# Optimization experiments

Measured on AMD Instinct MI355X. Metric: run time of the kernel, lower is better.

Reference implementation:

```python
import jax, jax.numpy as jnp
import numpy as np
from jax.scipy.special import logsumexp

EPS = 0.05        # entropic regularization (blur^p)
N_ITERS = 20      # Sinkhorn iterations
N, M, D = 8192, 8192, 64


def setup_inputs() -> dict:
    key = jax.random.key(0)
    k1, k2, k3, k4 = jax.random.split(key, 4)
    return {
        "a": jax.random.uniform(k1, (N,), dtype=jnp.float32),
        "x": jax.random.normal(k2, (N, D), dtype=jnp.float32),
        "b": jax.random.uniform(k3, (M,), dtype=jnp.float32),
        "y": jax.random.normal(k4, (M, D), dtype=jnp.float32),
    }


def reference(a, x, b, y):
    eps = EPS
    # _normalize_weights: probability simplex
    a = a / jnp.sum(a)
    b = b / jnp.sum(b)
    loga = jnp.log(a)
    logb = jnp.log(b)
    # squared-Euclidean cost C_ij = ||x_i - y_j||^2, built via one GEMM (online kernel's math)
    x2 = jnp.sum(x * x, axis=1)            # [N]
    y2 = jnp.sum(y * y, axis=1)            # [M]
    C = x2[:, None] + y2[None, :] - 2.0 * (x @ y.T)   # [N, M]

    # log-domain Sinkhorn: f_i = -eps * LSE_j( log b_j + (g_j - C_ij)/eps )
    def softmin_rows(g_, C_, logw):   # reduce over columns j -> [N]
        return -eps * logsumexp(logw[None, :] + (g_[None, :] - C_) / eps, axis=1)

    def softmin_cols(f_, C_, logw):   # reduce over rows i -> [M]
        return -eps * logsumexp(logw[:, None] + (f_[:, None] - C_) / eps, axis=0)

    def body(i, fg):
        f_, g_ = fg
        f_ = softmin_rows(g_, C, logb)
        g_ = softmin_cols(f_, C, loga)
        return (f_, g_)

    f0 = jnp.zeros_like(a)
    g0 = jnp.zeros_like(b)
    f, g = jax.lax.fori_loop(0, N_ITERS, body, (f0, g0))

    # GeomLoss-style: one final symmetric update from detached potentials (Danskin)
    f_d = jax.lax.stop_gradient(f)
    g_d = jax.lax.stop_gradient(g)
    f_fin = softmin_rows(g_d, C, logb)
    g_fin = softmin_cols(f_d, C, loga)
    # OT_eps(a, b) = <a, f> + <b, g>
    return jnp.sum(a * f_fin) + jnp.sum(b * g_fin)
```

## Files before the change

### kernel.cpp

```cpp
#include <hip/hip_runtime.h>
#include <hip/hip_bf16.h>

#define EPS       0.05f
#define N_ITERS   20
#define NR        8192
#define DIM       64
#define LOG2E     1.4426950408889634f
#define LN2       0.6931471805599453f
#define S2        (2.0f * LOG2E / EPS)
#define EPSLN2    (EPS * LN2)
#define NEGINF    (-1e30f)
#define NSPLIT    4

typedef __attribute__((ext_vector_type(8))) short short8;
typedef __attribute__((ext_vector_type(4))) float float4v;

__device__ __forceinline__ float wave_reduce_sum(float v) {
    #pragma unroll
    for (int m = 1; m < 64; m <<= 1) v += __shfl_xor(v, m, 64);
    return v;
}

__device__ __forceinline__ float merge4_l(float2 p0, float2 p1, float2 p2, float2 p3) {
    float M = fmaxf(fmaxf(p0.x, p1.x), fmaxf(p2.x, p3.x));
    float S = p0.y * __builtin_amdgcn_exp2f(p0.x - M)
            + p1.y * __builtin_amdgcn_exp2f(p1.x - M)
            + p2.y * __builtin_amdgcn_exp2f(p2.x - M)
            + p3.y * __builtin_amdgcn_exp2f(p3.x - M);
    return M + __builtin_amdgcn_logf(S);
}

__global__ void sums_kernel(const float* __restrict__ a, const float* __restrict__ b,
                            float* __restrict__ sums) {
    __shared__ float red[32];
    int tid = threadIdx.x;
    float pa = 0.f, pb = 0.f;
    for (int i = tid; i < NR; i += blockDim.x) { pa += a[i]; pb += b[i]; }
    pa = wave_reduce_sum(pa);
    pb = wave_reduce_sum(pb);
    int wid = tid >> 6, ln = tid & 63;
    if (ln == 0) { red[wid] = pa; red[wid + 16] = pb; }
    __syncthreads();
    if (tid == 0) {
        float sa = 0.f, sb = 0.f;
        int nw = blockDim.x >> 6;
        for (int w = 0; w < nw; w++) { sa += red[w]; sb += red[w + 16]; }
        sums[0] = logf(sa); sums[1] = logf(sb); sums[2] = sa; sums[3] = sb;
    }
}

__global__ void prep_kernel(const float* __restrict__ x, const float* __restrict__ y,
                            const float* __restrict__ a, const float* __restrict__ b,
                            const float* __restrict__ sums,
                            short8* __restrict__ xr, short8* __restrict__ yr,
                            short8* __restrict__ xs, short8* __restrict__ ys,
                            float* __restrict__ x2, float* __restrict__ y2,
                            float* __restrict__ la2, float* __restrict__ lb2,
                            float2* __restrict__ Pb) {
    int gid = blockIdx.x * 256 + threadIdx.x;
    bool isx = gid < NR * 8;
    int cid = isx ? gid : gid - NR * 8;
    int row = cid >> 3;
    int c   = cid & 7;
    const float4* src = (const float4*)(isx ? x : y);
    float4 v0 = src[row * 16 + c * 2];
    float4 v1 = src[row * 16 + c * 2 + 1];

    short8 st;
    st[0] = __bfloat16_as_short(__float2bfloat16(v0.x));
    st[1] = __bfloat16_as_short(__float2bfloat16(v0.y));
    st[2] = __bfloat16_as_short(__float2bfloat16(v0.z));
    st[3] = __bfloat16_as_short(__float2bfloat16(v0.w));
    st[4] = __bfloat16_as_short(__float2bfloat16(v1.x));
    st[5] = __bfloat16_as_short(__float2bfloat16(v1.y));
    st[6] = __bfloat16_as_short(__float2bfloat16(v1.z));
    st[7] = __bfloat16_as_short(__float2bfloat16(v1.w));

    (isx ? xr : yr)[row * 8 + c] = st;
    int T = row >> 4, ln = row & 15, f = c >> 2, q = c & 3;
    (isx ? xs : ys)[T * 128 + f * 64 + q * 16 + ln] = st;

    float sq = v0.x*v0.x + v0.y*v0.y + v0.z*v0.z + v0.w*v0.w
             + v1.x*v1.x + v1.y*v1.y + v1.z*v1.z + v1.w*v1.w;
    #pragma unroll
    for (int m = 1; m < 8; m <<= 1) sq += __shfl_xor(sq, m, 64);

    if (c == 0) {
        if (isx) {
            x2[row] = sq;
            la2[row] = (logf(a[row]) - sums[0]) * LOG2E;
        } else {
            y2[row] = sq;
            lb2[row] = (logf(b[row]) - sums[1]) * LOG2E;
            Pb[row] = make_float2(sq * (LOG2E / EPS), 1.0f);
            #pragma unroll
            for (int k = 1; k < NSPLIT; k++)
                Pb[k * NR + row] = make_float2(NEGINF, 0.0f);
        }
    }
}

#define LSE4(acc, c4, mm, ss)                                            \
    {                                                                    \
        float z0 = fmaf(S2, (acc)[0], (c4).x);                           \
        float z1 = fmaf(S2, (acc)[1], (c4).y);                           \
        float z2 = fmaf(S2, (acc)[2], (c4).z);                           \
        float z3 = fmaf(S2, (acc)[3], (c4).w);                           \
        float zm = fmaxf(fmaxf(z0, z1), fmaxf(z2, z3));                  \
        float mn = fmaxf((mm), zm);                                      \
        float e  = __builtin_amdgcn_exp2f((mm) - mn);                    \
        float p  = (__builtin_amdgcn_exp2f(z0 - mn)                      \
                  + __builtin_amdgcn_exp2f(z1 - mn))                     \
                 + (__builtin_amdgcn_exp2f(z2 - mn)                      \
                  + __builtin_amdgcn_exp2f(z3 - mn));                    \
        (ss) = fmaf((ss), e, p);                                         \
        (mm) = mn;                                                       \
    }

__global__ __launch_bounds__(1024, 4) void pass_kernel(
        const short8* __restrict__ matXr,
        const short8* __restrict__ matYs,
        const float2* __restrict__ Pin,
        const float* __restrict__ lw2col,
        float2* __restrict__ Pout) {
    __shared__ __attribute__((aligned(16))) char ybuf[2][32768];
    __shared__ __attribute__((aligned(16))) float cbl[2048];
    __shared__ float2 comb[128][9];

    const int tid = threadIdx.x;
    const int bi  = blockIdx.x;
    const int q4  = bi & 3;
    const int rb  = (bi >> 2) * 128;
    const int cb0 = q4 * 2048;

    {
        int j = cb0 + tid * 2;
        float4 p0 = *(const float4*)(Pin + 0 * NR + j);
        float4 p1 = *(const float4*)(Pin + 1 * NR + j);
        float4 p2 = *(const float4*)(Pin + 2 * NR + j);
        float4 p3 = *(const float4*)(Pin + 3 * NR + j);
        float2 lw = *(const float2*)(lw2col + j);
        float2 cb;
        cb.x = lw.x - merge4_l(make_float2(p0.x, p0.y), make_float2(p1.x, p1.y),
                               make_float2(p2.x, p2.y), make_float2(p3.x, p3.y));
        cb.y = lw.y - merge4_l(make_float2(p0.z, p0.w), make_float2(p1.z, p1.w),
                               make_float2(p2.z, p2.w), make_float2(p3.z, p3.w));
        *(float2*)(cbl + tid * 2) = cb;
    }

    const int w    = tid >> 6;
    const int lane = tid & 63;
    const int quad = lane >> 4;
    const int ln   = lane & 15;
    const int cs   = w & 7;
    const int rh   = w >> 3;

    short8 xf0[4], xf1[4];
    #pragma unroll
    for (int t = 0; t < 4; t++) {
        int r = rb + rh * 64 + t * 16 + ln;
        xf0[t] = matXr[r * 8 + quad];
        xf1[t] = matXr[r * 8 + quad + 4];
    }

    const char* ysrc = (const char*)matYs + (size_t)cb0 * 128;
    const int s0 = (bi >> 2) & 7;

    {
        const char* src = ysrc + s0 * 32768 + tid * 16;
        char* dst = &ybuf[0][(tid >> 6) * 1024];
        __builtin_amdgcn_global_load_lds(
            (const __attribute__((address_space(1))) void*)src,
            (__attribute__((address_space(3))) void*)dst, 16, 0, 0);
        __builtin_amdgcn_global_load_lds(
            (const __attribute__((address_space(1))) void*)(src + 16384),
            (__attribute__((address_space(3))) void*)(dst + 16384), 16, 0, 0);
    }

    float lm[4], ls[4];
    #pragma unroll
    for (int t = 0; t < 4; t++) { lm[t] = NEGINF; ls[t] = 0.f; }

    for (int t = 0; t < 8; t++) {
        const int cur = t & 1;
        const int sc  = (s0 + t) & 7;

        __builtin_amdgcn_s_waitcnt(0x0070);
        __builtin_amdgcn_s_barrier();
        __builtin_amdgcn_sched_barrier(0);

        if (t < 7) {
            const int sn = (s0 + t + 1) & 7;
            const char* src = ysrc + sn * 32768 + tid * 16;
            char* dst = &ybuf[1 - cur][(tid >> 6) * 1024];
            __builtin_amdgcn_global_load_lds(
                (const __attribute__((address_space(1))) void*)src,
                (__attribute__((address_space(3))) void*)dst, 16, 0, 0);
            __builtin_amdgcn_global_load_lds(
                (const __attribute__((address_space(1))) void*)(src + 16384),
                (__attribute__((address_space(3))) void*)(dst + 16384), 16, 0, 0);
        }
        __builtin_amdgcn_sched_barrier(0);

        const char* base = &ybuf[cur][0];
        #pragma unroll
        for (int uu = 0; uu < 2; uu++) {
            const int u = 2 * cs + uu;
            short8 ya0 = *(const short8*)(base + u * 2048 + lane * 16);
            short8 ya1 = *(const short8*)(base + u * 2048 + 1024 + lane * 16);
            float4 c4  = *(const float4*)(cbl + sc * 256 + u * 16 + quad * 4);

            float4v acc[4];
            #pragma unroll
            for (int tt = 0; tt < 4; tt++) {
                float4v z = {0.f, 0.f, 0.f, 0.f};
                z = __builtin_amdgcn_mfma_f32_16x16x32_bf16(ya0, xf0[tt], z, 0, 0, 0);
                z = __builtin_amdgcn_mfma_f32_16x16x32_bf16(ya1, xf1[tt], z, 0, 0, 0);
                acc[tt] = z;
            }
            #pragma unroll
            for (int tt = 0; tt < 4; tt++) LSE4(acc[tt], c4, lm[tt], ls[tt]);
        }
    }

    #pragma unroll
    for (int mask = 16; mask < 64; mask <<= 1) {
        #pragma unroll
        for (int t = 0; t < 4; t++) {
            float mo = __shfl_xor(lm[t], mask, 64);
            float so = __shfl_xor(ls[t], mask, 64);
            float M  = fmaxf(lm[t], mo);
            ls[t] = ls[t] * __builtin_amdgcn_exp2f(lm[t] - M)
                  + so    * __builtin_amdgcn_exp2f(mo    - M);
            lm[t] = M;
        }
    }

    if (lane < 16) {
        #pragma unroll
        for (int t = 0; t < 4; t++)
            comb[rh * 64 + t * 16 + ln][cs] = make_float2(lm[t], ls[t]);
    }
    __syncthreads();

    if (tid < 128) {
        float2 c = comb[tid][0];
        float M = c.x, S = c.y;
        #pragma unroll
        for (int cc = 1; cc < 8; cc++) {
            float2 p = comb[tid][cc];
            float Mn = fmaxf(M, p.x);
            S = S * __builtin_amdgcn_exp2f(M - Mn)
              + p.y * __builtin_amdgcn_exp2f(p.x - Mn);
            M = Mn;
        }
        Pout[q4 * NR + rb + tid] = make_float2(M, S);
    }
}

__global__ void reduce_kernel(const float* __restrict__ a, const float* __restrict__ b,
                              const float* __restrict__ sums,
                              const float* __restrict__ x2, const float* __restrict__ y2,
                              const float2* __restrict__ Pff, const float2* __restrict__ Pgf,
                              float* __restrict__ out) {
    __shared__ float red[32];
    int tid = threadIdx.x;
    float da = 0.f, db = 0.f;
    for (int i = tid; i < NR; i += blockDim.x) {
        float fv = x2[i] - EPSLN2 * merge4_l(Pff[i], Pff[NR + i],
                                             Pff[2 * NR + i], Pff[3 * NR + i]);
        float gv = y2[i] - EPSLN2 * merge4_l(Pgf[i], Pgf[NR + i],
                                             Pgf[2 * NR + i], Pgf[3 * NR + i]);
        da += a[i] * fv;
        db += b[i] * gv;
    }
    da = wave_reduce_sum(da);
    db = wave_reduce_sum(db);
    int wid = tid >> 6, ln = tid & 63;
    if (ln == 0) { red[wid] = da; red[wid + 16] = db; }
    __syncthreads();
    if (tid == 0) {
        float DA = 0.f, DB = 0.f;
        int nw = blockDim.x >> 6;
        for (int w = 0; w < nw; w++) { DA += red[w]; DB += red[w + 16]; }
        out[0] = DA / sums[2] + DB / sums[3];
    }
}

extern "C" void kernel_launch(void* const* d_in, const int* in_sizes, int n_in,
                              void* d_out, int out_size, void* d_ws, size_t ws_size,
                              hipStream_t stream) {
    const float* a = (const float*)d_in[0];
    const float* x = (const float*)d_in[1];
    const float* b = (const float*)d_in[2];
    const float* y = (const float*)d_in[3];

    char* ws = (char*)d_ws;
    short8* xr = (short8*)ws;
    short8* yr = (short8*)(ws + (1 << 20));
    short8* xs = (short8*)(ws + (2 << 20));
    short8* ys = (short8*)(ws + (3 << 20));
    float* fp  = (float*)(ws + (4 << 20));
    float* x2  = fp;
    float* y2  = fp + NR;
    float* la2 = fp + 2 * NR;
    float* lb2 = fp + 3 * NR;
    float2* P   = (float2*)(fp + 4 * NR);
    float2* Pf  = P;
    float2* Pb  = P + NSPLIT * NR;
    float2* Pff = P + 2 * NSPLIT * NR;
    float2* Pgf = P + 3 * NSPLIT * NR;
    float* sums = (float*)(P + 4 * NSPLIT * NR);

    sums_kernel<<<1, 1024, 0, stream>>>(a, b, sums);
    prep_kernel<<<(2 * NR * 8) / 256, 256, 0, stream>>>(x, y, a, b, sums,
                                                        xr, yr, xs, ys,
                                                        x2, y2, la2, lb2, Pb);

    for (int it = 0; it < N_ITERS; it++) {
        pass_kernel<<<256, 1024, 0, stream>>>(xr, ys, Pb, lb2, Pf);
        pass_kernel<<<256, 1024, 0, stream>>>(yr, xs, Pf, la2, Pb);
    }
    pass_kernel<<<256, 1024, 0, stream>>>(xr, ys, Pb, lb2, Pff);
    pass_kernel<<<256, 1024, 0, stream>>>(yr, xs, Pf, la2, Pgf);

    reduce_kernel<<<1, 1024, 0, stream>>>(a, b, sums, x2, y2, Pff, Pgf, (float*)d_out);
}
```

Measured before the change: 974.1 us.

## Retile pass kernel to 256-row blocks with 8-way column split and triple-buffered Y

Each pass block now covers 256 rows and a 1024-column slice, giving an 8-way column split instead of 4. This doubles the X-fragment reuse per wave and halves the Y bytes staged per step, and the Y loads become a three-deep LDS ring with one load kept in flight. The work is meant to raise MFMA work per LDS read and to hide global-load latency better. In exchange it costs more registers (8 row tiles of accumulators and LSE state) and doubles the partial-LSE merge work, both in the pass prologue and in the final reduce. The host launch grid is not shown and must match the new block count.

New measurement: 1.160 ms. +19.1%, slower.

```diff
diff --git a/kernel.cpp b/kernel.cpp
--- a/kernel.cpp
+++ b/kernel.cpp
@@ -10,24 +10,20 @@
 #define S2        (2.0f * LOG2E / EPS)
 #define EPSLN2    (EPS * LN2)
 #define NEGINF    (-1e30f)
-#define NSPLIT    4
+#define NSPLIT    8
 
 typedef __attribute__((ext_vector_type(8))) short short8;
 typedef __attribute__((ext_vector_type(4))) float float4v;
 
+#define GLD_LDS16(src, dst)                                              \
+    __builtin_amdgcn_global_load_lds(                                    \
+        (const __attribute__((address_space(1))) void*)(src),            \
+        (__attribute__((address_space(3))) void*)(dst), 16, 0, 0)
+
 __device__ __forceinline__ float wave_reduce_sum(float v) {
     #pragma unroll
     for (int m = 1; m < 64; m <<= 1) v += __shfl_xor(v, m, 64);
     return v;
-}
-
-__device__ __forceinline__ float merge4_l(float2 p0, float2 p1, float2 p2, float2 p3) {
-    float M = fmaxf(fmaxf(p0.x, p1.x), fmaxf(p2.x, p3.x));
-    float S = p0.y * __builtin_amdgcn_exp2f(p0.x - M)
-            + p1.y * __builtin_amdgcn_exp2f(p1.x - M)
-            + p2.y * __builtin_amdgcn_exp2f(p2.x - M)
-            + p3.y * __builtin_amdgcn_exp2f(p3.x - M);
-    return M + __builtin_amdgcn_logf(S);
 }
 
 __global__ void sums_kernel(const float* __restrict__ a, const float* __restrict__ b,
@@ -123,30 +119,16 @@
         const float2* __restrict__ Pin,
         const float* __restrict__ lw2col,
         float2* __restrict__ Pout) {
-    __shared__ __attribute__((aligned(16))) char ybuf[2][32768];
-    __shared__ __attribute__((aligned(16))) float cbl[2048];
-    __shared__ float2 comb[128][9];
+    __shared__ __attribute__((aligned(16))) char ybuf[3][16384];
+    __shared__ __attribute__((aligned(16))) float cbl[1024];
+    __shared__ float2 comb[256][9];
 
     const int tid = threadIdx.x;
     const int bi  = blockIdx.x;
-    const int q4  = bi & 3;
-    const int rb  = (bi >> 2) * 128;
-    const int cb0 = q4 * 2048;
-
-    {
-        int j = cb0 + tid * 2;
-        float4 p0 = *(const float4*)(Pin + 0 * NR + j);
-        float4 p1 = *(const float4*)(Pin + 1 * NR + j);
-        float4 p2 = *(const float4*)(Pin + 2 * NR + j);
-        float4 p3 = *(const float4*)(Pin + 3 * NR + j);
-        float2 lw = *(const float2*)(lw2col + j);
-        float2 cb;
-        cb.x = lw.x - merge4_l(make_float2(p0.x, p0.y), make_float2(p1.x, p1.y),
-                               make_float2(p2.x, p2.y), make_float2(p3.x, p3.y));
-        cb.y = lw.y - merge4_l(make_float2(p0.z, p0.w), make_float2(p1.z, p1.w),
-                               make_float2(p2.z, p2.w), make_float2(p3.z, p3.w));
-        *(float2*)(cbl + tid * 2) = cb;
-    }
+    const int q8  = bi & 7;
+    const int rg  = bi >> 3;
+    const int rb  = rg * 256;
+    const int cb0 = q8 * 1024;
 
     const int w    = tid >> 6;
     const int lane = tid & 63;
@@ -155,78 +137,76 @@
     const int cs   = w & 7;
     const int rh   = w >> 3;
 
-    short8 xf0[4], xf1[4];
-    #pragma unroll
-    for (int t = 0; t < 4; t++) {
-        int r = rb + rh * 64 + t * 16 + ln;
+    const char* ysrc = (const char*)matYs + (size_t)cb0 * 128;
+    const int c0 = rg & 7;
+
+    GLD_LDS16(ysrc + c0 * 16384 + w * 1024 + lane * 16, &ybuf[0][w * 1024]);
+    __builtin_amdgcn_sched_barrier(0);
+
+    {
+        int j = cb0 + tid;
+        float2 p[NSPLIT];
+        float M = NEGINF;
+        #pragma unroll
+        for (int k = 0; k < NSPLIT; k++) {
+            p[k] = Pin[k * NR + j];
+            M = fmaxf(M, p[k].x);
+        }
+        float S = 0.f;
+        #pragma unroll
+        for (int k = 0; k < NSPLIT; k++)
+            S += p[k].y * __builtin_amdgcn_exp2f(p[k].x - M);
+        cbl[tid] = lw2col[j] - (M + __builtin_amdgcn_logf(S));
+    }
+
+    short8 xf0[8], xf1[8];
+    #pragma unroll
+    for (int t = 0; t < 8; t++) {
+        int r = rb + rh * 128 + t * 16 + ln;
         xf0[t] = matXr[r * 8 + quad];
         xf1[t] = matXr[r * 8 + quad + 4];
     }
 
-    const char* ysrc = (const char*)matYs + (size_t)cb0 * 128;
-    const int s0 = (bi >> 2) & 7;
-
-    {
-        const char* src = ysrc + s0 * 32768 + tid * 16;
-        char* dst = &ybuf[0][(tid >> 6) * 1024];
-        __builtin_amdgcn_global_load_lds(
-            (const __attribute__((address_space(1))) void*)src,
-            (__attribute__((address_space(3))) void*)dst, 16, 0, 0);
-        __builtin_amdgcn_global_load_lds(
-            (const __attribute__((address_space(1))) void*)(src + 16384),
-            (__attribute__((address_space(3))) void*)(dst + 16384), 16, 0, 0);
-    }
-
-    float lm[4], ls[4];
-    #pragma unroll
-    for (int t = 0; t < 4; t++) { lm[t] = NEGINF; ls[t] = 0.f; }
-
+    __builtin_amdgcn_sched_barrier(0);
+    GLD_LDS16(ysrc + ((c0 + 1) & 7) * 16384 + w * 1024 + lane * 16, &ybuf[1][w * 1024]);
+    __builtin_amdgcn_sched_barrier(0);
+
+    float lm[8], ls[8];
+    #pragma unroll
+    for (int t = 0; t < 8; t++) { lm[t] = NEGINF; ls[t] = 0.f; }
+
+    #pragma unroll
     for (int t = 0; t < 8; t++) {
-        const int cur = t & 1;
-        const int sc  = (s0 + t) & 7;
-
-        __builtin_amdgcn_s_waitcnt(0x0070);
+        if (t < 7) __builtin_amdgcn_s_waitcnt(0x0071);
+        else       __builtin_amdgcn_s_waitcnt(0x0070);
         __builtin_amdgcn_s_barrier();
         __builtin_amdgcn_sched_barrier(0);
 
-        if (t < 7) {
-            const int sn = (s0 + t + 1) & 7;
-            const char* src = ysrc + sn * 32768 + tid * 16;
-            char* dst = &ybuf[1 - cur][(tid >> 6) * 1024];
-            __builtin_amdgcn_global_load_lds(
-                (const __attribute__((address_space(1))) void*)src,
-                (__attribute__((address_space(3))) void*)dst, 16, 0, 0);
-            __builtin_amdgcn_global_load_lds(
-                (const __attribute__((address_space(1))) void*)(src + 16384),
-                (__attribute__((address_space(3))) void*)(dst + 16384), 16, 0, 0);
+        if (t < 6) {
+            GLD_LDS16(ysrc + ((c0 + t + 2) & 7) * 16384 + w * 1024 + lane * 16,
+                      &ybuf[(t + 2) % 3][w * 1024]);
         }
         __builtin_amdgcn_sched_barrier(0);
 
-        const char* base = &ybuf[cur][0];
-        #pragma unroll
-        for (int uu = 0; uu < 2; uu++) {
-            const int u = 2 * cs + uu;
-            short8 ya0 = *(const short8*)(base + u * 2048 + lane * 16);
-            short8 ya1 = *(const short8*)(base + u * 2048 + 1024 + lane * 16);
-            float4 c4  = *(const float4*)(cbl + sc * 256 + u * 16 + quad * 4);
-
-            float4v acc[4];
-            #pragma unroll
-            for (int tt = 0; tt < 4; tt++) {
-                float4v z = {0.f, 0.f, 0.f, 0.f};
-                z = __builtin_amdgcn_mfma_f32_16x16x32_bf16(ya0, xf0[tt], z, 0, 0, 0);
-                z = __builtin_amdgcn_mfma_f32_16x16x32_bf16(ya1, xf1[tt], z, 0, 0, 0);
-                acc[tt] = z;
-            }
-            #pragma unroll
-            for (int tt = 0; tt < 4; tt++) LSE4(acc[tt], c4, lm[tt], ls[tt]);
+        const int  sc   = (c0 + t) & 7;
+        const char* base = &ybuf[t % 3][0];
+        short8 ya0 = *(const short8*)(base + cs * 2048 + lane * 16);
+        short8 ya1 = *(const short8*)(base + cs * 2048 + 1024 + lane * 16);
+        float4 c4  = *(const float4*)(cbl + sc * 128 + cs * 16 + quad * 4);
+
+        #pragma unroll
+        for (int tt = 0; tt < 8; tt++) {
+            float4v acc = {0.f, 0.f, 0.f, 0.f};
+            acc = __builtin_amdgcn_mfma_f32_16x16x32_bf16(ya0, xf0[tt], acc, 0, 0, 0);
+            acc = __builtin_amdgcn_mfma_f32_16x16x32_bf16(ya1, xf1[tt], acc, 0, 0, 0);
+            LSE4(acc, c4, lm[tt], ls[tt]);
         }
     }
 
     #pragma unroll
     for (int mask = 16; mask < 64; mask <<= 1) {
         #pragma unroll
-        for (int t = 0; t < 4; t++) {
+        for (int t = 0; t < 8; t++) {
             float mo = __shfl_xor(lm[t], mask, 64);
             float so = __shfl_xor(ls[t], mask, 64);
             float M  = fmaxf(lm[t], mo);
@@ -238,12 +218,12 @@
 
     if (lane < 16) {
         #pragma unroll
-        for (int t = 0; t < 4; t++)
-            comb[rh * 64 + t * 16 + ln][cs] = make_float2(lm[t], ls[t]);
+        for (int t = 0; t < 8; t++)
+            comb[rh * 128 + t * 16 + ln][cs] = make_float2(lm[t], ls[t]);
     }
     __syncthreads();
 
-    if (tid < 128) {
+    if (tid < 256) {
         float2 c = comb[tid][0];
         float M = c.x, S = c.y;
         #pragma unroll
@@ -254,8 +234,23 @@
               + p.y * __builtin_amdgcn_exp2f(p.x - Mn);
             M = Mn;
         }
-        Pout[q4 * NR + rb + tid] = make_float2(M, S);
-    }
+        Pout[q8 * NR + rb + tid] = make_float2(M, S);
+    }
+}
+
+__device__ __forceinline__ float merge8_full(const float2* __restrict__ P, int i) {
+    float2 p[NSPLIT];
+    float M = NEGINF;
+    #pragma unroll
+    for (int k = 0; k < NSPLIT; k++) {
+        p[k] = P[k * NR + i];
+        M = fmaxf(M, p[k].x);
+    }
+    float S = 0.f;
+    #pragma unroll
+    for (int k = 0; k < NSPLIT; k++)
+        S += p[k].y * __builtin_amdgcn_exp2f(p[k].x - M);
+    return M + __builtin_amdgcn_logf(S);
 }
 
 __global__ void reduce_kernel(const float* __restrict__ a, const float* __restrict__ b,
@@ -267,10 +262,8 @@
     int tid = threadIdx.x;
     float da = 0.f, db = 0.f;
     for (int i = tid; i < NR; i += blockDim.x) {
-        float fv = x2[i] - EPSLN2 * merge4_l(Pff[i], Pff[NR + i],
-                                             Pff[2 * NR + i], Pff[3 * NR + i]);
-        float gv = y2[i] - EPSLN2 * merge4_l(Pgf[i], Pgf[NR + i],
-                                             Pgf[2 * NR + i], Pgf[3 * NR + i]);
+        float fv = x2[i] - EPSLN2 * merge8_full(Pff, i);
+        float gv = y2[i] - EPSLN2 * merge8_full(Pgf, i);
         da += a[i] * fv;
         db += b[i] * gv;
     }
```
